# Kernel optimization log

Hardware: AMD Instinct MI355X
Metric: run time of the kernel (lower is better)

## Reference

```python
import jax, jax.numpy as jnp
import numpy as np

EMBED = 1024
HEADS = 16
HEAD_DIM = EMBED // HEADS
OUT = 1024


def setup_inputs() -> dict:
    key = jax.random.key(0)
    ks = jax.random.split(key, 6)
    x = jax.random.normal(ks[0], (4, 2048, EMBED), dtype=jnp.float32)
    # per-head projection weights, torch Linear convention: [out_features, in_features]
    s = 1.0 / np.sqrt(HEAD_DIM)
    Wv = jax.random.uniform(ks[1], (HEAD_DIM, HEAD_DIM), jnp.float32, -s, s)
    Wk = jax.random.uniform(ks[2], (HEAD_DIM, HEAD_DIM), jnp.float32, -s, s)
    Wq = jax.random.uniform(ks[3], (HEAD_DIM, HEAD_DIM), jnp.float32, -s, s)
    so = 1.0 / np.sqrt(EMBED)
    Wo = jax.random.uniform(ks[4], (OUT, EMBED), jnp.float32, -so, so)
    bo = jax.random.uniform(ks[5], (OUT,), jnp.float32, -so, so)
    return {"x": x, "Wq": Wq, "Wk": Wk, "Wv": Wv, "Wo": Wo, "bo": bo}


def reference(x, Wq, Wk, Wv, Wo, bo):
    N, L, _ = x.shape
    xh = x.reshape(N, L, HEADS, HEAD_DIM)  # nqhd
    q = jnp.einsum('nqhd,ed->nqhe', xh, Wq)
    k = jnp.einsum('nkhd,ed->nkhe', xh, Wk)
    v = jnp.einsum('nkhd,ed->nkhe', xh, Wv)
    # full score matrix [N, H, Q, K], scaled by sqrt(embed_size) as in source
    energy = jnp.einsum('nqhd,nkhd->nhqk', q, k) / np.sqrt(EMBED).astype(np.float32)
    attn = jax.nn.softmax(energy, axis=3)
    out = jnp.einsum('nhqk,nkhd->nqhd', attn, v).reshape(N, L, EMBED)
    return out @ Wo.T + bo
```

## Files before the change

### kernel.cpp

```cpp
#include <hip/hip_runtime.h>
#include <hip/hip_bf16.h>
#include <stdint.h>
#include <stddef.h>


typedef __attribute__((ext_vector_type(8))) short bf16x8;
typedef __attribute__((ext_vector_type(4))) float f32x4;
typedef __attribute__((ext_vector_type(4))) short short4v;
typedef __attribute__((ext_vector_type(2))) uint32_t uint2v;

__device__ __forceinline__ f32x4 mfma16(bf16x8 a, bf16x8 b, f32x4 c) {
    return __builtin_amdgcn_mfma_f32_16x16x32_bf16(a, b, c, 0, 0, 0);
}

__device__ __forceinline__ short f2bf(float x) {
    union { float f; uint32_t u; } v; v.f = x;
    uint32_t r = (v.u + 0x7FFFu + ((v.u >> 16) & 1u)) >> 16;
    return (short)(uint16_t)r;
}

__device__ __forceinline__ uint32_t pk2bf(float a, float b) {
    union { __hip_bfloat162 h; uint32_t u; } v;
    v.h = __float22bfloat162_rn(float2{a, b});
    return v.u;
}

__device__ __forceinline__ bf16x8 cvt8(const float* __restrict__ p) {
    f32x4 a = *(const f32x4*)p;
    f32x4 b = *(const f32x4*)(p + 4);
    bf16x8 r;
    r[0] = f2bf(a[0]); r[1] = f2bf(a[1]); r[2] = f2bf(a[2]); r[3] = f2bf(a[3]);
    r[4] = f2bf(b[0]); r[5] = f2bf(b[1]); r[6] = f2bf(b[2]); r[7] = f2bf(b[3]);
    return r;
}

__global__ __launch_bounds__(256)
void wpack_kernel(const float* __restrict__ Wo, const float* __restrict__ Wq,
                  const float* __restrict__ Wk, const float* __restrict__ Wv,
                  short* __restrict__ wo_f, short* __restrict__ wqkv_f) {
    int b = blockIdx.x;
    if (b < 512) {
        int idx = b * 256 + threadIdx.x;
        int nrow = idx >> 7;
        int k0 = (idx & 127) * 8;
        bf16x8 v = cvt8(Wo + (size_t)nrow * 1024 + k0);
        int ntile = nrow >> 4, lcn = nrow & 15;
        int kseg = k0 >> 5, qd = (k0 >> 3) & 3;
        *(bf16x8*)(wo_f + ((size_t)(ntile * 32 + kseg) * 64 + qd * 16 + lcn) * 8) = v;
    } else {
        const float* W = (b == 512) ? Wq : (b == 513) ? Wk : Wv;
        short* dst = wqkv_f + (size_t)(b - 512) * 4096;
        for (int u = threadIdx.x; u < 512; u += 256) {
            int seg = u >> 6, ln = u & 63;
            int nt = seg >> 1, kf = seg & 1, lq = ln >> 4, lcn = ln & 15;
            bf16x8 v = cvt8(W + (nt * 16 + lcn) * 64 + kf * 32 + lq * 8);
            *(bf16x8*)(dst + u * 8) = v;
        }
    }
}

__global__ __launch_bounds__(256)
void kvproj_kernel(const float* __restrict__ x, const short* __restrict__ wqkv_f,
                   short* __restrict__ kf_ws, short* __restrict__ vf_ws) {
    __shared__ alignas(16) short kbuf[128 * 72];
    __shared__ alignas(16) short vbuf[64 * 136];
    int tid = threadIdx.x;
    int lt = blockIdx.x & 15, nh = blockIdx.x >> 4;
    int n = nh >> 4, h = nh & 15;
    int l0 = lt * 128, kt0 = lt * 2;
    int wv = tid >> 6, lane = tid & 63, quad = lane >> 4, lc = lane & 15;
    const short* wkf = wqkv_f + 4096 + lane * 8;
    const short* wvf = wqkv_f + 8192 + lane * 8;

    for (int u = tid; u < 1024; u += 256) {
        int r = u >> 3, c = (u & 7) * 8;
        *(bf16x8*)(kbuf + r * 72 + c) =
            cvt8(x + (size_t)(n * 2048 + l0 + r) * 1024 + h * 64 + c);
    }
    __syncthreads();

    bf16x8 xa[2][2];
    for (int mt = 0; mt < 2; ++mt)
        for (int kf = 0; kf < 2; ++kf)
            xa[mt][kf] = *(bf16x8*)(kbuf + (wv * 32 + mt * 16 + lc) * 72 + kf * 32 + quad * 8);

    f32x4 ka[2][4] = {}, va[2][4] = {};
    for (int nt = 0; nt < 4; ++nt)
        for (int kf = 0; kf < 2; ++kf) {
            bf16x8 wkb = *(const bf16x8*)(wkf + (nt * 2 + kf) * 512);
            bf16x8 wvb = *(const bf16x8*)(wvf + (nt * 2 + kf) * 512);
            for (int mt = 0; mt < 2; ++mt) {
                ka[mt][nt] = mfma16(xa[mt][kf], wkb, ka[mt][nt]);
                va[mt][nt] = mfma16(xa[mt][kf], wvb, va[mt][nt]);
            }
        }

    for (int mt = 0; mt < 2; ++mt) {
        int off = wv * 32 + mt * 16;
        for (int nt = 0; nt < 4; ++nt) {
            short4v pv;
            for (int i = 0; i < 4; ++i) {
                kbuf[(off + quad * 4 + i) * 72 + nt * 16 + lc] = f2bf(ka[mt][nt][i]);
                pv[i] = f2bf(va[mt][nt][i]);
            }
            *(short4v*)(vbuf + (nt * 16 + lc) * 136 + off + quad * 4) = pv;
        }
    }
    __syncthreads();

    size_t base = (size_t)nh * 131072 + (size_t)kt0 * 4096;
    for (int u = tid; u < 1024; u += 256) {
        int tile = u >> 9, rem = u & 511, seg = rem >> 6, ln = u & 63;
        int t = seg >> 1, kf = seg & 1;
        int lq = ln >> 4, ll = ln & 15;
        bf16x8 kw = *(bf16x8*)(kbuf + (tile * 64 + t * 16 + ll) * 72 + kf * 32 + lq * 8);
        *(bf16x8*)(kf_ws + base + (size_t)tile * 4096 + seg * 512 + ln * 8) = kw;
        bf16x8 vw = *(bf16x8*)(vbuf + (t * 16 + ll) * 136 + tile * 64 + kf * 32 + lq * 8);
        *(bf16x8*)(vf_ws + base + (size_t)tile * 4096 + seg * 512 + ln * 8) = vw;
    }
}

__global__ __launch_bounds__(256, 2)
void flash_kernel(const float* __restrict__ x, const short* __restrict__ wqkv_f,
                  const short* __restrict__ kf_ws, const short* __restrict__ vf_ws,
                  short* __restrict__ ao) {
    __shared__ alignas(16) short pbuf[256 * 72];
    int tid = threadIdx.x;
    int nh = blockIdx.x & 63, qt = blockIdx.x >> 6;
    int n = nh >> 4, h = nh & 15;
    int q0 = qt * 256;
    int wv = tid >> 6, lane = tid & 63, quad = lane >> 4, lc = lane & 15;

    for (int u = tid; u < 2048; u += 256) {
        int r = u >> 3, c = (u & 7) * 8;
        *(bf16x8*)(pbuf + r * 72 + c) =
            cvt8(x + (size_t)(n * 2048 + q0 + r) * 1024 + h * 64 + c);
    }
    __syncthreads();
    {
        const short* wqf = wqkv_f + lane * 8;
        bf16x8 xa[4][2];
        for (int mt = 0; mt < 4; ++mt)
            for (int kf = 0; kf < 2; ++kf)
                xa[mt][kf] = *(bf16x8*)(pbuf + (wv * 64 + mt * 16 + lc) * 72 +
                                        kf * 32 + quad * 8);
        f32x4 qacc[4][4] = {};
        for (int nt = 0; nt < 4; ++nt)
            for (int kf = 0; kf < 2; ++kf) {
                bf16x8 wb = *(const bf16x8*)(wqf + (nt * 2 + kf) * 512);
                for (int mt = 0; mt < 4; ++mt)
                    qacc[mt][nt] = mfma16(xa[mt][kf], wb, qacc[mt][nt]);
            }
        const float QS = 0.04508422002778011f;
        for (int mt = 0; mt < 4; ++mt)
            for (int nt = 0; nt < 4; ++nt)
                for (int i = 0; i < 4; ++i)
                    pbuf[(wv * 64 + mt * 16 + quad * 4 + i) * 72 + nt * 16 + lc] =
                        f2bf(qacc[mt][nt][i] * QS);
    }
    bf16x8 qa[4][2];
    for (int mt = 0; mt < 4; ++mt)
        for (int kf = 0; kf < 2; ++kf)
            qa[mt][kf] = *(bf16x8*)(pbuf + (wv * 64 + mt * 16 + lc) * 72 +
                                    kf * 32 + quad * 8);

    f32x4 o[4][4] = {};
    float lsum[4] = {0.f, 0.f, 0.f, 0.f};
    const short* kbase = kf_ws + (size_t)nh * 131072 + lane * 8;
    const short* vbase = vf_ws + (size_t)nh * 131072 + lane * 8;

    for (int kt = 0; kt < 32; ++kt) {
        const short* kp = kbase + (size_t)kt * 4096;
        const short* vp = vbase + (size_t)kt * 4096;
        bf16x8 vA[4][2];
#pragma unroll
        for (int dt = 0; dt < 4; ++dt)
            for (int kf = 0; kf < 2; ++kf)
                vA[dt][kf] = *(const bf16x8*)(vp + (dt * 2 + kf) * 512);

#pragma unroll
        for (int t = 0; t < 4; ++t) {
            bf16x8 k0 = *(const bf16x8*)(kp + (t * 2 + 0) * 512);
            bf16x8 k1 = *(const bf16x8*)(kp + (t * 2 + 1) * 512);
            f32x4 s[4];
#pragma unroll
            for (int q2 = 0; q2 < 4; ++q2) {
                f32x4 acc = {};
                acc = mfma16(k0, qa[q2][0], acc);
                acc = mfma16(k1, qa[q2][1], acc);
                s[q2] = acc;
            }
#pragma unroll
            for (int q2 = 0; q2 < 4; ++q2) {
                float p0 = __builtin_amdgcn_exp2f(s[q2][0]);
                float p1 = __builtin_amdgcn_exp2f(s[q2][1]);
                float p2 = __builtin_amdgcn_exp2f(s[q2][2]);
                float p3 = __builtin_amdgcn_exp2f(s[q2][3]);
                lsum[q2] += (p0 + p1) + (p2 + p3);
                uint2v w = {pk2bf(p0, p1), pk2bf(p2, p3)};
                *(uint2v*)(pbuf + (wv * 64 + q2 * 16 + lc) * 72 + t * 16 + quad * 4) = w;
            }
        }

#pragma unroll
        for (int q2 = 0; q2 < 4; ++q2)
            for (int kf = 0; kf < 2; ++kf) {
                bf16x8 pB = *(bf16x8*)(pbuf + (wv * 64 + q2 * 16 + lc) * 72 +
                                       kf * 32 + quad * 8);
                for (int dt = 0; dt < 4; ++dt)
                    o[q2][dt] = mfma16(vA[dt][kf], pB, o[q2][dt]);
            }
    }

    for (int q2 = 0; q2 < 4; ++q2) {
        float t = lsum[q2];
        t += __shfl_xor(t, 16, 64);
        t += __shfl_xor(t, 32, 64);
        float inv = 1.f / t;
        int mtile = (n * 2048 + q0) / 16 + wv * 4 + q2;
        for (int dt = 0; dt < 4; ++dt) {
            int kseg = h * 2 + (dt >> 1);
            int qd8 = ((dt & 1) * 4 + quad) >> 1;
            short4v pk;
            for (int i = 0; i < 4; ++i) pk[i] = f2bf(o[q2][dt][i] * inv);
            *(short4v*)(ao + (size_t)(mtile * 32 + kseg) * 512 +
                        (qd8 * 16 + lc) * 8 + (quad & 1) * 4) = pk;
        }
    }
}

__global__ __launch_bounds__(256)
void outgemm_kernel(const short* __restrict__ afb, const short* __restrict__ wfb,
                    const float* __restrict__ bo, float* __restrict__ out) {
    int tid = threadIdx.x;
    int bm = blockIdx.x & 63, bn = blockIdx.x >> 6;
    int m0 = bm * 128, n0 = bn * 128;
    int wv = tid >> 6, lane = tid & 63, quad = lane >> 4, lc = lane & 15;
    int wr = wv >> 1, wc = wv & 1;
    int mtb = bm * 8 + wr * 4;
    int ntb = bn * 8 + wc * 4;

    const short* ab = afb + lane * 8;
    const short* bb = wfb + lane * 8;

    f32x4 acc[4][4] = {};
    for (int kt = 0; kt < 32; ++kt) {
        bf16x8 af[4], bfr[4];
#pragma unroll
        for (int mt = 0; mt < 4; ++mt)
            af[mt] = *(const bf16x8*)(ab + ((size_t)(mtb + mt) * 32 + kt) * 512);
#pragma unroll
        for (int nt = 0; nt < 4; ++nt)
            bfr[nt] = *(const bf16x8*)(bb + ((size_t)(ntb + nt) * 32 + kt) * 512);
#pragma unroll
        for (int mt = 0; mt < 4; ++mt)
            for (int nt = 0; nt < 4; ++nt)
                acc[mt][nt] = mfma16(af[mt], bfr[nt], acc[mt][nt]);
    }
    for (int nt = 0; nt < 4; ++nt) {
        float bv = bo[n0 + wc * 64 + nt * 16 + lc];
        for (int mt = 0; mt < 4; ++mt)
            for (int i = 0; i < 4; ++i) {
                int m = m0 + wr * 64 + mt * 16 + quad * 4 + i;
                int nn = n0 + wc * 64 + nt * 16 + lc;
                out[(size_t)m * 1024 + nn] = acc[mt][nt][i] + bv;
            }
    }
}

extern "C" void kernel_launch(void* const* d_in, const int* in_sizes, int n_in,
                              void* d_out, int out_size, void* d_ws, size_t ws_size,
                              hipStream_t stream) {
    const float* x  = (const float*)d_in[0];
    const float* Wq = (const float*)d_in[1];
    const float* Wk = (const float*)d_in[2];
    const float* Wv = (const float*)d_in[3];
    const float* Wo = (const float*)d_in[4];
    const float* bo = (const float*)d_in[5];
    float* out = (float*)d_out;

    short* kf_ws   = (short*)d_ws;
    short* vf_ws   = kf_ws + 8388608;
    short* ao_ws   = vf_ws + 8388608;
    short* wo_f    = ao_ws + 8388608;
    short* wqkv_f  = wo_f + 1048576;

    wpack_kernel<<<dim3(515), dim3(256), 0, stream>>>(Wo, Wq, Wk, Wv, wo_f, wqkv_f);
    kvproj_kernel<<<dim3(1024), dim3(256), 0, stream>>>(x, wqkv_f, kf_ws, vf_ws);
    flash_kernel<<<dim3(512), dim3(256), 0, stream>>>(x, wqkv_f, kf_ws, vf_ws, ao_ws);
    outgemm_kernel<<<dim3(512), dim3(256), 0, stream>>>(ao_ws, wo_f, bo, out);
}
```

Measured before the change: 217.3 us.

## Keep softmax probabilities in registers using permlane16 swap instead of LDS

Instead of writing the exponentiated scores to shared memory and reading them back as MFMA B-operands, the kernel packs them to bf16 in registers and rearranges lanes with permlane16_swap, falling back to shuffles when the builtin is unavailable. The V workspace layout is permuted on the producer side to match the new register fragment order. K and V loads for each tile are hoisted together, and the loop is reordered per query subtile. This removes LDS round-trips and the associated waits in the inner loop, at the cost of more live registers and cross-lane permute instructions. A __syncthreads is also added after the Q projection.

```diff
diff --git a/kernel.cpp b/kernel.cpp
--- a/kernel.cpp
+++ b/kernel.cpp
@@ -32,6 +32,20 @@
     r[0] = f2bf(a[0]); r[1] = f2bf(a[1]); r[2] = f2bf(a[2]); r[3] = f2bf(a[3]);
     r[4] = f2bf(b[0]); r[5] = f2bf(b[1]); r[6] = f2bf(b[2]); r[7] = f2bf(b[3]);
     return r;
+}
+
+__device__ __forceinline__ void swap16(uint32_t a, uint32_t b,
+                                       uint32_t& lo, uint32_t& hi) {
+#if __has_builtin(__builtin_amdgcn_permlane16_swap)
+    uint2v r = __builtin_amdgcn_permlane16_swap(a, b, false, false);
+    lo = r[0]; hi = r[1];
+#else
+    int lane = (int)(threadIdx.x & 63);
+    uint32_t bl = (uint32_t)__shfl((int)b, lane & 47);
+    uint32_t ah = (uint32_t)__shfl((int)a, lane | 16);
+    lo = (lane & 16) ? bl : a;
+    hi = (lane & 16) ? b : ah;
+#endif
 }
 
 __global__ __launch_bounds__(256)
@@ -113,9 +127,10 @@
         int tile = u >> 9, rem = u & 511, seg = rem >> 6, ln = u & 63;
         int t = seg >> 1, kf = seg & 1;
         int lq = ln >> 4, ll = ln & 15;
+        int bq = ((lq & 1) << 1) | (lq >> 1);
         bf16x8 kw = *(bf16x8*)(kbuf + (tile * 64 + t * 16 + ll) * 72 + kf * 32 + lq * 8);
         *(bf16x8*)(kf_ws + base + (size_t)tile * 4096 + seg * 512 + ln * 8) = kw;
-        bf16x8 vw = *(bf16x8*)(vbuf + (t * 16 + ll) * 136 + tile * 64 + kf * 32 + lq * 8);
+        bf16x8 vw = *(bf16x8*)(vbuf + (t * 16 + ll) * 136 + tile * 64 + kf * 32 + bq * 8);
         *(bf16x8*)(vf_ws + base + (size_t)tile * 4096 + seg * 512 + ln * 8) = vw;
     }
 }
@@ -158,6 +173,7 @@
                     pbuf[(wv * 64 + mt * 16 + quad * 4 + i) * 72 + nt * 16 + lc] =
                         f2bf(qacc[mt][nt][i] * QS);
     }
+    __syncthreads();
     bf16x8 qa[4][2];
     for (int mt = 0; mt < 4; ++mt)
         for (int kf = 0; kf < 2; ++kf)
@@ -172,44 +188,49 @@
     for (int kt = 0; kt < 32; ++kt) {
         const short* kp = kbase + (size_t)kt * 4096;
         const short* vp = vbase + (size_t)kt * 4096;
-        bf16x8 vA[4][2];
-#pragma unroll
-        for (int dt = 0; dt < 4; ++dt)
-            for (int kf = 0; kf < 2; ++kf)
-                vA[dt][kf] = *(const bf16x8*)(vp + (dt * 2 + kf) * 512);
-
-#pragma unroll
-        for (int t = 0; t < 4; ++t) {
-            bf16x8 k0 = *(const bf16x8*)(kp + (t * 2 + 0) * 512);
-            bf16x8 k1 = *(const bf16x8*)(kp + (t * 2 + 1) * 512);
+        bf16x8 kA[4][2], vA[4][2];
+#pragma unroll
+        for (int t = 0; t < 4; ++t)
+            for (int kf = 0; kf < 2; ++kf) {
+                kA[t][kf] = *(const bf16x8*)(kp + (t * 2 + kf) * 512);
+                vA[t][kf] = *(const bf16x8*)(vp + (t * 2 + kf) * 512);
+            }
+
+#pragma unroll
+        for (int q2 = 0; q2 < 4; ++q2) {
             f32x4 s[4];
 #pragma unroll
-            for (int q2 = 0; q2 < 4; ++q2) {
+            for (int t = 0; t < 4; ++t) {
                 f32x4 acc = {};
-                acc = mfma16(k0, qa[q2][0], acc);
-                acc = mfma16(k1, qa[q2][1], acc);
-                s[q2] = acc;
-            }
-#pragma unroll
-            for (int q2 = 0; q2 < 4; ++q2) {
-                float p0 = __builtin_amdgcn_exp2f(s[q2][0]);
-                float p1 = __builtin_amdgcn_exp2f(s[q2][1]);
-                float p2 = __builtin_amdgcn_exp2f(s[q2][2]);
-                float p3 = __builtin_amdgcn_exp2f(s[q2][3]);
-                lsum[q2] += (p0 + p1) + (p2 + p3);
-                uint2v w = {pk2bf(p0, p1), pk2bf(p2, p3)};
-                *(uint2v*)(pbuf + (wv * 64 + q2 * 16 + lc) * 72 + t * 16 + quad * 4) = w;
-            }
-        }
-
-#pragma unroll
-        for (int q2 = 0; q2 < 4; ++q2)
+                acc = mfma16(kA[t][0], qa[q2][0], acc);
+                acc = mfma16(kA[t][1], qa[q2][1], acc);
+                s[t] = acc;
+            }
+            uint32_t p0[4], p1[4];
+            float ts = 0.f;
+#pragma unroll
+            for (int t = 0; t < 4; ++t) {
+                float e0 = __builtin_amdgcn_exp2f(s[t][0]);
+                float e1 = __builtin_amdgcn_exp2f(s[t][1]);
+                float e2 = __builtin_amdgcn_exp2f(s[t][2]);
+                float e3 = __builtin_amdgcn_exp2f(s[t][3]);
+                ts += (e0 + e1) + (e2 + e3);
+                p0[t] = pk2bf(e0, e1);
+                p1[t] = pk2bf(e2, e3);
+            }
+            lsum[q2] += ts;
+#pragma unroll
             for (int kf = 0; kf < 2; ++kf) {
-                bf16x8 pB = *(bf16x8*)(pbuf + (wv * 64 + q2 * 16 + lc) * 72 +
-                                       kf * 32 + quad * 8);
+                uint32_t r0, r1, r2, r3;
+                swap16(p0[2 * kf], p0[2 * kf + 1], r0, r2);
+                swap16(p1[2 * kf], p1[2 * kf + 1], r1, r3);
+                union { uint32_t u[4]; bf16x8 v; } fr;
+                fr.u[0] = r0; fr.u[1] = r1; fr.u[2] = r2; fr.u[3] = r3;
+#pragma unroll
                 for (int dt = 0; dt < 4; ++dt)
-                    o[q2][dt] = mfma16(vA[dt][kf], pB, o[q2][dt]);
-            }
+                    o[q2][dt] = mfma16(vA[dt][kf], fr.v, o[q2][dt]);
+            }
+        }
     }
 
     for (int q2 = 0; q2 < 4; ++q2) {
```

Measured after the change: 203.3 us. -6.4%, faster.
